# Kernel tuning notes

Measured on AMD Instinct MI355X. Metric: run time of the kernel, lower is better.

Reference implementation:

```python
import jax, jax.numpy as jnp
import numpy as np

B, D_IN, D_HID, D_OUT, N_EXP, K = 32768, 256, 512, 256, 16, 2


def setup_inputs() -> dict:
    key = jax.random.key(0)
    ks = jax.random.split(key, 5)
    s_in = 1.0 / np.sqrt(D_IN)
    s_hid = 1.0 / np.sqrt(D_HID)
    return {
        "x": jax.random.normal(ks[0], (B, D_IN), jnp.float32),
        "Wg": jax.random.normal(ks[1], (D_IN, N_EXP), jnp.float32) * s_in,
        "bg": jnp.zeros((N_EXP,), jnp.float32),
        "W1": jax.random.normal(ks[2], (N_EXP, D_IN, D_HID), jnp.float32) * s_in,
        "b1": jnp.zeros((N_EXP, D_HID), jnp.float32),
        "W2": jax.random.normal(ks[3], (N_EXP, D_HID, D_OUT), jnp.float32) * s_hid,
        "b2": jnp.zeros((N_EXP, D_OUT), jnp.float32),
    }


def reference(x, Wg, bg, W1, b1, W2, b2):
    # Gating: linear -> softmax -> top-k -> renormalize (inference path, no noise)
    logits = x @ Wg + bg                       # [B, E]
    probs = jax.nn.softmax(logits, axis=-1)
    top_w, top_idx = jax.lax.top_k(probs, K)   # [B, K]
    top_w = top_w / jnp.sum(top_w, axis=-1, keepdims=True)

    # Expert MLPs (evaluate all experts densely, then gather selected outputs;
    # same math as masked gather -> MLP -> weighted scatter-add)
    h = jax.nn.relu(jnp.einsum('bi,eih->beh', x, W1) + b1[None])  # [B, E, H]
    y_all = jnp.einsum('beh,eho->beo', h, W2) + b2[None]          # [B, E, O]

    y_sel = jnp.take_along_axis(y_all, top_idx[:, :, None], axis=1)  # [B, K, O]
    return jnp.sum(y_sel * top_w[:, :, None], axis=1)                # [B, O]
```

## Files before the change

### kernel.cpp

```cpp
#include <hip/hip_runtime.h>
#include <stdint.h>

#define BTOK 32768
#define DIN 256
#define DHID 512
#define DOUT 256
#define NEXP 16
#define BM 128
#define CH 32
#define NCH 16
#define SLOTS 96

typedef __attribute__((ext_vector_type(8))) short bf16x8;
typedef __attribute__((ext_vector_type(4))) float f32x4;

__device__ __forceinline__ unsigned short f2bf(float f){
  unsigned u = __builtin_bit_cast(unsigned, f);
  u = u + 0x7FFFu + ((u >> 16) & 1u);
  return (unsigned short)(u >> 16);
}
__device__ __forceinline__ float bf2f(unsigned short h){
  return __builtin_bit_cast(float, (unsigned)h << 16);
}
__device__ __forceinline__ void gload16(const void* g, void* l){
  __builtin_amdgcn_global_load_lds((const __attribute__((address_space(1))) unsigned int*)g,
                                   (__attribute__((address_space(3))) unsigned int*)l, 16, 0, 0);
}

__global__ __launch_bounds__(256) void transpose_cvt(const float* __restrict__ src,
                                                     unsigned short* __restrict__ dst,
                                                     int R, int C){
  __shared__ float t[32][33];
  int e = blockIdx.z, r0 = blockIdx.y * 32, c0 = blockIdx.x * 32;
  int lx = threadIdx.x & 31, ly = threadIdx.x >> 5;
  const float* s = src + (size_t)e * R * C;
  unsigned short* d = dst + (size_t)e * R * C;
#pragma unroll
  for (int i = 0; i < 4; i++){ int r = ly + i * 8; t[r][lx] = s[(size_t)(r0 + r) * C + c0 + lx]; }
  __syncthreads();
#pragma unroll
  for (int i = 0; i < 4; i++){ int r = ly + i * 8; d[(size_t)(c0 + r) * R + r0 + lx] = f2bf(t[lx][r]); }
}

__global__ __launch_bounds__(256) void transpose_cvt_w2(const float* __restrict__ src,
                                                        unsigned short* __restrict__ dst){
  __shared__ float t[32][33];
  int e = blockIdx.z, r0 = blockIdx.y * 32, c0 = blockIdx.x * 32;
  int lx = threadIdx.x & 31, ly = threadIdx.x >> 5;
  const float* s = src + (size_t)e * DHID * DOUT;
  unsigned short* d = dst + (size_t)e * DHID * DOUT + (r0 >> 5) * (DOUT * CH);
#pragma unroll
  for (int i = 0; i < 4; i++){ int r = ly + i * 8; t[r][lx] = s[(size_t)(r0 + r) * DOUT + c0 + lx]; }
  __syncthreads();
#pragma unroll
  for (int i = 0; i < 4; i++){ int rr = ly + i * 8; d[(size_t)(c0 + rr) * CH + lx] = f2bf(t[lx][rr]); }
}

__global__ __launch_bounds__(256) void gating_kernel(const float* __restrict__ x,
                                                     const float* __restrict__ Wg,
                                                     const float* __restrict__ bg,
                                                     unsigned short* __restrict__ x_bf,
                                                     int* __restrict__ top_idx,
                                                     float* __restrict__ top_w,
                                                     int* __restrict__ counts){
  __shared__ float WgT[16][256];
  __shared__ int hist[16];
  int tid = threadIdx.x;
#pragma unroll
  for (int j = 0; j < 4; j++){
    float4 wv = *(const float4*)(Wg + tid * 16 + j * 4);
    WgT[j * 4 + 0][tid] = wv.x; WgT[j * 4 + 1][tid] = wv.y;
    WgT[j * 4 + 2][tid] = wv.z; WgT[j * 4 + 3][tid] = wv.w;
  }
  if (tid < 16) hist[tid] = 0;
  __syncthreads();
  int wid = tid >> 6, lane = tid & 63;

  for (int t = 0; t < 16; t++){
    int tok = blockIdx.x * 64 + wid * 16 + t;
    const float4 xv = *(const float4*)(x + (size_t)tok * DIN + lane * 4);
    ushort4 xb; xb.x = f2bf(xv.x); xb.y = f2bf(xv.y); xb.z = f2bf(xv.z); xb.w = f2bf(xv.w);
    *(ushort4*)(x_bf + (size_t)tok * DIN + lane * 4) = xb;
    float logit[16];
#pragma unroll
    for (int e = 0; e < 16; e++){
      const float4 wv = *(const float4*)(&WgT[e][lane * 4]);
      float v = xv.x * wv.x + xv.y * wv.y + xv.z * wv.z + xv.w * wv.w;
#pragma unroll
      for (int off = 32; off; off >>= 1) v += __shfl_xor(v, off, 64);
      logit[e] = v + bg[e];
    }
    if (lane == 0){
      int i1 = 0; float v1 = logit[0];
#pragma unroll
      for (int e = 1; e < 16; e++) if (logit[e] > v1){ v1 = logit[e]; i1 = e; }
      int i2 = -1; float v2 = -3.4e38f;
#pragma unroll
      for (int e = 0; e < 16; e++) if (e != i1 && logit[e] > v2){ v2 = logit[e]; i2 = e; }
      float tt = expf(v2 - v1);
      float w1 = 1.0f / (1.0f + tt);
      float w2 = tt / (1.0f + tt);
      top_idx[tok * 2] = i1; top_idx[tok * 2 + 1] = i2;
      top_w[tok * 2] = w1;  top_w[tok * 2 + 1] = w2;
      atomicAdd(&hist[i1], 1); atomicAdd(&hist[i2], 1);
    }
  }
  __syncthreads();
  if (tid < 16) atomicAdd(&counts[tid], hist[tid]);
}

__global__ void prefix_kernel(const int* __restrict__ counts, int* __restrict__ offsets,
                              int* __restrict__ cursor, int* __restrict__ bm_e,
                              int* __restrict__ bm_start, int* __restrict__ bm_end){
  int lane = threadIdx.x & 63;
  int c = (lane < 16) ? counts[lane] : 0;
  int s = c;
#pragma unroll
  for (int off = 1; off < 16; off <<= 1){ int o = __shfl_up(s, off, 64); if (lane >= off) s += o; }
  int start = s - c;
  if (lane < 16){ offsets[lane] = start; cursor[lane] = start; }
  int nb = (c + BM - 1) >> 7;
  int nb_partner = __shfl(nb, lane ^ 8, 64);
  if (lane < 8){
    int filled = nb + nb_partner;
    if (filled > SLOTS) filled = SLOTS;
    for (int i = filled; i < SLOTS; i++) bm_e[lane * SLOTS + i] = -1;
  }
  if (lane < 16){
    int sbase = (lane < 8) ? 0 : nb_partner;
    int xcd = lane & 7;
    for (int b = 0; b < nb; b++){
      int idx = xcd * SLOTS + sbase + b;
      if (sbase + b < SLOTS){
        bm_e[idx] = lane; bm_start[idx] = start + b * BM; bm_end[idx] = start + c;
      }
    }
  }
}

__global__ __launch_bounds__(256) void scatter_kernel(const int* __restrict__ top_idx,
                                                      const float* __restrict__ top_w,
                                                      int* __restrict__ cursor,
                                                      int* __restrict__ pair_tok,
                                                      float* __restrict__ pair_w){
  __shared__ int hist[16], base[16], rank[16];
  int tid = threadIdx.x;
  if (tid < 16){ hist[tid] = 0; rank[tid] = 0; }
  __syncthreads();
  int t = blockIdx.x * 256 + tid;
  int e0 = top_idx[t * 2], e1 = top_idx[t * 2 + 1];
  float w0 = top_w[t * 2], w1 = top_w[t * 2 + 1];
  atomicAdd(&hist[e0], 1); atomicAdd(&hist[e1], 1);
  __syncthreads();
  if (tid < 16) base[tid] = atomicAdd(&cursor[tid], hist[tid]);
  __syncthreads();
  int r0 = atomicAdd(&rank[e0], 1);
  int p0 = base[e0] + r0;
  pair_tok[p0] = t; pair_w[p0] = w0;
  int r1 = atomicAdd(&rank[e1], 1);
  int p1 = base[e1] + r1;
  pair_tok[p1] = t | (1 << 16); pair_w[p1] = w1;
}

__global__ __launch_bounds__(512, 1) void moe_gemm_kernel(
    const unsigned short* __restrict__ x_bf,
    const unsigned short* __restrict__ W1t,
    const unsigned short* __restrict__ W2c,
    const float* __restrict__ b1,
    const float* __restrict__ b2,
    const int* __restrict__ pair_tok, const float* __restrict__ pair_w,
    const int* __restrict__ bm_e, const int* __restrict__ bm_start,
    const int* __restrict__ bm_end,
    unsigned short* __restrict__ ypair){
  int xcd = blockIdx.x & 7, slot = blockIdx.x >> 3;
  int bmi = xcd * SLOTS + slot;
  int e = bm_e[bmi];
  if (e < 0) return;
  int rs = bm_start[bmi], re = bm_end[bmi];

  __shared__ unsigned short w1s[3][CH * 256];
  __shared__ unsigned short w2s[3][256 * CH];
  __shared__ unsigned short hs[BM * CH];
  __shared__ float b1s[DHID];

  int tid = threadIdx.x, wid = tid >> 6, lane = tid & 63, lr = lane & 15, lh = lane >> 4;
  int mg = wid >> 1, ng = wid & 1;
  char* hsb = (char*)hs;
  const char* gW1 = (const char*)(W1t + (size_t)e * DHID * DIN);
  const char* gW2 = (const char*)(W2c + (size_t)e * DOUT * DHID);

  b1s[tid] = b1[e * DHID + tid];

  int o1 = ((tid >> 5) * 512) + (((tid & 31) ^ ((tid >> 5) & 7)) * 16);
  int o2;
  { int p = tid >> 3, q = (tid & 7) ^ (p & 7);
    o2 = (p * 2 + (q >> 2)) * 64 + (q & 3) * 16; }

#define STAGE(c, sl) {                                                    \
    const char* s1 = gW1 + (size_t)(c) * 16384;                           \
    const char* s2 = gW2 + (size_t)(c) * 16384;                           \
    char* d1 = (char*)w1s[sl]; char* d2 = (char*)w2s[sl];                 \
    gload16(s1 + o1,        d1 + tid * 16);                               \
    gload16(s1 + o1 + 8192, d1 + tid * 16 + 8192);                        \
    gload16(s2 + o2,        d2 + tid * 16);                               \
    gload16(s2 + o2 + 8192, d2 + tid * 16 + 8192);                        \
  }

  bf16x8 xr[2][8];
#pragma unroll
  for (int m = 0; m < 2; m++){
    int g0 = rs + 32 * mg + m * 16 + lr;
    int gc = g0 < re ? g0 : (re - 1);
    int tok = pair_tok[gc] & 0xFFFF;
    const unsigned short* xrow = x_bf + (size_t)tok * DIN + lh * 8;
#pragma unroll
    for (int ks = 0; ks < 8; ks++) xr[m][ks] = *(const bf16x8*)(xrow + ks * 32);
  }

  f32x4 acc[2][8];
#pragma unroll
  for (int m = 0; m < 2; m++)
#pragma unroll
    for (int i = 0; i < 8; i++) acc[m][i] = (f32x4){0.f, 0.f, 0.f, 0.f};

  STAGE(0, 0); STAGE(1, 1);
  __syncthreads();

#pragma unroll 1
  for (int c = 0; c < NCH; c++){
    int b0 = c % 3;
    if (c + 2 < NCH) STAGE(c + 2, (c + 2) % 3);

    {
      const char* w1b = (const char*)w1s[b0];
      f32x4 hacc[2];
      hacc[0] = (f32x4){0.f, 0.f, 0.f, 0.f};
      hacc[1] = (f32x4){0.f, 0.f, 0.f, 0.f};
      int hrow = 16 * ng + lr;
#pragma unroll
      for (int ks = 0; ks < 8; ks++){
        bf16x8 b = *(const bf16x8*)(w1b + ((hrow * 512 + ks * 64 + lh * 16) ^ ((hrow & 7) << 4)));
        hacc[0] = __builtin_amdgcn_mfma_f32_16x16x32_bf16(xr[0][ks], b, hacc[0], 0, 0, 0);
        hacc[1] = __builtin_amdgcn_mfma_f32_16x16x32_bf16(xr[1][ks], b, hacc[1], 0, 0, 0);
      }
      float b1v = b1s[c * CH + 16 * ng + lr];
      int col2 = (16 * ng + lr) * 2;
#pragma unroll
      for (int m = 0; m < 2; m++)
#pragma unroll
        for (int r = 0; r < 4; r++){
          int mm = 32 * mg + m * 16 + lh * 4 + r;
          float v = fmaxf(hacc[m][r] + b1v, 0.f);
          int adr = (mm >> 1) * 128 + ((((mm & 1) << 6) + col2) ^ (((mm >> 1) & 7) << 4));
          *(unsigned short*)(hsb + adr) = f2bf(v);
        }
    }
    asm volatile("s_waitcnt lgkmcnt(0)" ::: "memory");
    __builtin_amdgcn_sched_barrier(0);
    __builtin_amdgcn_s_barrier();
    __builtin_amdgcn_sched_barrier(0);

    {
      const char* w2b = (const char*)w2s[b0];
      bf16x8 ha[2];
#pragma unroll
      for (int m = 0; m < 2; m++){
        int mm = 32 * mg + m * 16 + lr;
        int hadr = (mm >> 1) * 128 + ((((mm & 1) << 6) + (lh << 4)) ^ (((mm >> 1) & 7) << 4));
        ha[m] = *(const bf16x8*)(hsb + hadr);
      }
#pragma unroll
      for (int nt = 0; nt < 8; nt++){
        int n = 128 * ng + nt * 16 + lr;
        int adr = (n >> 1) * 128 + ((((n & 1) << 6) + (lh << 4)) ^ (((n >> 1) & 7) << 4));
        bf16x8 b = *(const bf16x8*)(w2b + adr);
        acc[0][nt] = __builtin_amdgcn_mfma_f32_16x16x32_bf16(ha[0], b, acc[0][nt], 0, 0, 0);
        acc[1][nt] = __builtin_amdgcn_mfma_f32_16x16x32_bf16(ha[1], b, acc[1][nt], 0, 0, 0);
      }
    }
    if (c + 1 < NCH){
      if (c + 2 < NCH){
        asm volatile("s_waitcnt vmcnt(4) lgkmcnt(0)" ::: "memory");
      } else {
        asm volatile("s_waitcnt vmcnt(0) lgkmcnt(0)" ::: "memory");
      }
      __builtin_amdgcn_sched_barrier(0);
      __builtin_amdgcn_s_barrier();
      __builtin_amdgcn_sched_barrier(0);
    }
  }

#pragma unroll
  for (int m = 0; m < 2; m++){
    float wrow[4]; int yrow[4]; int valid[4];
#pragma unroll
    for (int r = 0; r < 4; r++){
      int gg = rs + 32 * mg + m * 16 + lh * 4 + r;
      valid[r] = gg < re;
      int gc = valid[r] ? gg : (re - 1);
      int pt = pair_tok[gc];
      yrow[r] = (pt & 0xFFFF) * 2 + (pt >> 16);
      wrow[r] = valid[r] ? pair_w[gc] : 0.f;
    }
#pragma unroll
    for (int nt = 0; nt < 8; nt++){
      int col = 128 * ng + nt * 16 + lr;
      float b2v = b2[e * DOUT + col];
#pragma unroll
      for (int r = 0; r < 4; r++){
        if (valid[r])
          ypair[(size_t)yrow[r] * DOUT + col] = f2bf(wrow[r] * (acc[m][nt][r] + b2v));
      }
    }
  }
#undef STAGE
}

__global__ __launch_bounds__(256) void combine_kernel(const unsigned short* __restrict__ yp,
                                                      float* __restrict__ out){
  int idx = blockIdx.x * 256 + threadIdx.x;
  int t = idx >> 6;
  int c4 = (idx & 63) << 2;
  ushort4 a = *(const ushort4*)(yp + (size_t)(t * 2) * DOUT + c4);
  ushort4 b = *(const ushort4*)(yp + (size_t)(t * 2 + 1) * DOUT + c4);
  float4 o;
  o.x = bf2f(a.x) + bf2f(b.x);
  o.y = bf2f(a.y) + bf2f(b.y);
  o.z = bf2f(a.z) + bf2f(b.z);
  o.w = bf2f(a.w) + bf2f(b.w);
  *(float4*)(out + (size_t)t * DOUT + c4) = o;
}

extern "C" void kernel_launch(void* const* d_in, const int* in_sizes, int n_in,
                              void* d_out, int out_size, void* d_ws, size_t ws_size,
                              hipStream_t stream){
  (void)in_sizes; (void)n_in; (void)out_size; (void)ws_size;
  const float* x  = (const float*)d_in[0];
  const float* Wg = (const float*)d_in[1];
  const float* bg = (const float*)d_in[2];
  const float* W1 = (const float*)d_in[3];
  const float* b1 = (const float*)d_in[4];
  const float* W2 = (const float*)d_in[5];
  const float* b2 = (const float*)d_in[6];
  float* out = (float*)d_out;
  char* ws = (char*)d_ws;

  unsigned short* x_bf  = (unsigned short*)(ws);
  unsigned short* W1t   = (unsigned short*)(ws + 16777216);
  unsigned short* W2ck  = (unsigned short*)(ws + 20971520);
  unsigned short* ypair = (unsigned short*)(ws + 25165824);
  int*   top_idx  = (int*)  (ws + 58720256);
  float* top_w    = (float*)(ws + 58982400);
  int*   pair_tok = (int*)  (ws + 59244544);
  float* pair_w   = (float*)(ws + 59506688);
  int*   counts   = (int*)  (ws + 60030976);
  int*   offsets  = (int*)  (ws + 60031040);
  int*   cursor   = (int*)  (ws + 60031104);
  int*   bm_e     = (int*)  (ws + 60031232);
  int*   bm_start = (int*)  (ws + 60036608);
  int*   bm_end   = (int*)  (ws + 60041984);

  hipMemsetAsync(counts, 0, 64, stream);
  transpose_cvt<<<dim3(16, 8, 16), 256, 0, stream>>>(W1, W1t, 256, 512);
  transpose_cvt_w2<<<dim3(8, 16, 16), 256, 0, stream>>>(W2, W2ck);
  gating_kernel<<<512, 256, 0, stream>>>(x, Wg, bg, x_bf, top_idx, top_w, counts);
  prefix_kernel<<<1, 64, 0, stream>>>(counts, offsets, cursor, bm_e, bm_start, bm_end);
  scatter_kernel<<<128, 256, 0, stream>>>(top_idx, top_w, cursor, pair_tok, pair_w);
  moe_gemm_kernel<<<8 * SLOTS, 512, 0, stream>>>(x_bf, W1t, W2ck, b1, b2, pair_tok, pair_w,
                                                 bm_e, bm_start, bm_end, ypair);
  combine_kernel<<<8192, 256, 0, stream>>>(ypair, out);
}
```

Before: 174.2 us.

## Halve MoE GEMM row tile, double-buffer weights, and raise occupancy

Shrinks the per-block token tile from 128 to 64 rows and raises the slot count, so roughly twice as many blocks are launched. Launch bounds now allow 4 blocks per CU. Weight staging drops from triple to double buffering, and the b1 shared-memory copy is replaced with direct global reads, which cuts LDS and register use. The goal is more resident waves to hide latency, at the cost of each block reloading the full expert weights for half as many tokens, which doubles weight traffic through the cache. The hand-tuned waitcnt and barrier sequence is replaced by plain __syncthreads.

```diff
diff --git a/kernel.cpp b/kernel.cpp
--- a/kernel.cpp
+++ b/kernel.cpp
@@ -6,10 +6,10 @@
 #define DHID 512
 #define DOUT 256
 #define NEXP 16
-#define BM 128
+#define BM 64
 #define CH 32
 #define NCH 16
-#define SLOTS 96
+#define SLOTS 168
 
 typedef __attribute__((ext_vector_type(8))) short bf16x8;
 typedef __attribute__((ext_vector_type(4))) float f32x4;
@@ -119,7 +119,7 @@
   for (int off = 1; off < 16; off <<= 1){ int o = __shfl_up(s, off, 64); if (lane >= off) s += o; }
   int start = s - c;
   if (lane < 16){ offsets[lane] = start; cursor[lane] = start; }
-  int nb = (c + BM - 1) >> 7;
+  int nb = (c + BM - 1) >> 6;
   int nb_partner = __shfl(nb, lane ^ 8, 64);
   if (lane < 8){
     int filled = nb + nb_partner;
@@ -162,7 +162,7 @@
   pair_tok[p1] = t | (1 << 16); pair_w[p1] = w1;
 }
 
-__global__ __launch_bounds__(512, 1) void moe_gemm_kernel(
+__global__ __launch_bounds__(512, 4) void moe_gemm_kernel(
     const unsigned short* __restrict__ x_bf,
     const unsigned short* __restrict__ W1t,
     const unsigned short* __restrict__ W2c,
@@ -178,18 +178,15 @@
   if (e < 0) return;
   int rs = bm_start[bmi], re = bm_end[bmi];
 
-  __shared__ unsigned short w1s[3][CH * 256];
-  __shared__ unsigned short w2s[3][256 * CH];
+  __shared__ unsigned short w1s[2][CH * 256];
+  __shared__ unsigned short w2s[2][256 * CH];
   __shared__ unsigned short hs[BM * CH];
-  __shared__ float b1s[DHID];
 
   int tid = threadIdx.x, wid = tid >> 6, lane = tid & 63, lr = lane & 15, lh = lane >> 4;
   int mg = wid >> 1, ng = wid & 1;
   char* hsb = (char*)hs;
   const char* gW1 = (const char*)(W1t + (size_t)e * DHID * DIN);
   const char* gW2 = (const char*)(W2c + (size_t)e * DOUT * DHID);
-
-  b1s[tid] = b1[e * DHID + tid];
 
   int o1 = ((tid >> 5) * 512) + (((tid & 31) ^ ((tid >> 5) & 7)) * 16);
   int o2;
@@ -206,96 +203,69 @@
     gload16(s2 + o2 + 8192, d2 + tid * 16 + 8192);                        \
   }
 
-  bf16x8 xr[2][8];
-#pragma unroll
-  for (int m = 0; m < 2; m++){
-    int g0 = rs + 32 * mg + m * 16 + lr;
+  bf16x8 xr[8];
+  {
+    int g0 = rs + 16 * mg + lr;
     int gc = g0 < re ? g0 : (re - 1);
     int tok = pair_tok[gc] & 0xFFFF;
     const unsigned short* xrow = x_bf + (size_t)tok * DIN + lh * 8;
 #pragma unroll
-    for (int ks = 0; ks < 8; ks++) xr[m][ks] = *(const bf16x8*)(xrow + ks * 32);
-  }
-
-  f32x4 acc[2][8];
-#pragma unroll
-  for (int m = 0; m < 2; m++)
-#pragma unroll
-    for (int i = 0; i < 8; i++) acc[m][i] = (f32x4){0.f, 0.f, 0.f, 0.f};
-
-  STAGE(0, 0); STAGE(1, 1);
-  __syncthreads();
-
-#pragma unroll 1
+    for (int ks = 0; ks < 8; ks++) xr[ks] = *(const bf16x8*)(xrow + ks * 32);
+  }
+
+  f32x4 acc[8];
+#pragma unroll
+  for (int i = 0; i < 8; i++) acc[i] = (f32x4){0.f, 0.f, 0.f, 0.f};
+
+  STAGE(0, 0);
+  __syncthreads();
+
   for (int c = 0; c < NCH; c++){
-    int b0 = c % 3;
-    if (c + 2 < NCH) STAGE(c + 2, (c + 2) % 3);
+    int sl = c & 1;
+    if (c + 1 < NCH) STAGE(c + 1, sl ^ 1);
 
     {
-      const char* w1b = (const char*)w1s[b0];
-      f32x4 hacc[2];
-      hacc[0] = (f32x4){0.f, 0.f, 0.f, 0.f};
-      hacc[1] = (f32x4){0.f, 0.f, 0.f, 0.f};
+      const char* w1b = (const char*)w1s[sl];
+      f32x4 hacc = (f32x4){0.f, 0.f, 0.f, 0.f};
       int hrow = 16 * ng + lr;
 #pragma unroll
       for (int ks = 0; ks < 8; ks++){
         bf16x8 b = *(const bf16x8*)(w1b + ((hrow * 512 + ks * 64 + lh * 16) ^ ((hrow & 7) << 4)));
-        hacc[0] = __builtin_amdgcn_mfma_f32_16x16x32_bf16(xr[0][ks], b, hacc[0], 0, 0, 0);
-        hacc[1] = __builtin_amdgcn_mfma_f32_16x16x32_bf16(xr[1][ks], b, hacc[1], 0, 0, 0);
-      }
-      float b1v = b1s[c * CH + 16 * ng + lr];
+        hacc = __builtin_amdgcn_mfma_f32_16x16x32_bf16(xr[ks], b, hacc, 0, 0, 0);
+      }
+      float b1v = b1[e * DHID + c * CH + 16 * ng + lr];
       int col2 = (16 * ng + lr) * 2;
 #pragma unroll
-      for (int m = 0; m < 2; m++)
-#pragma unroll
-        for (int r = 0; r < 4; r++){
-          int mm = 32 * mg + m * 16 + lh * 4 + r;
-          float v = fmaxf(hacc[m][r] + b1v, 0.f);
-          int adr = (mm >> 1) * 128 + ((((mm & 1) << 6) + col2) ^ (((mm >> 1) & 7) << 4));
-          *(unsigned short*)(hsb + adr) = f2bf(v);
-        }
-    }
-    asm volatile("s_waitcnt lgkmcnt(0)" ::: "memory");
-    __builtin_amdgcn_sched_barrier(0);
-    __builtin_amdgcn_s_barrier();
-    __builtin_amdgcn_sched_barrier(0);
+      for (int r = 0; r < 4; r++){
+        int mm = 16 * mg + lh * 4 + r;
+        float v = fmaxf(hacc[r] + b1v, 0.f);
+        int adr = (mm >> 1) * 128 + ((((mm & 1) << 6) + col2) ^ (((mm >> 1) & 7) << 4));
+        *(unsigned short*)(hsb + adr) = f2bf(v);
+      }
+    }
+    __syncthreads();
 
     {
-      const char* w2b = (const char*)w2s[b0];
-      bf16x8 ha[2];
-#pragma unroll
-      for (int m = 0; m < 2; m++){
-        int mm = 32 * mg + m * 16 + lr;
-        int hadr = (mm >> 1) * 128 + ((((mm & 1) << 6) + (lh << 4)) ^ (((mm >> 1) & 7) << 4));
-        ha[m] = *(const bf16x8*)(hsb + hadr);
-      }
+      int mm = 16 * mg + lr;
+      int hadr = (mm >> 1) * 128 + ((((mm & 1) << 6) + (lh << 4)) ^ (((mm >> 1) & 7) << 4));
+      bf16x8 ha = *(const bf16x8*)(hsb + hadr);
+      const char* w2b = (const char*)w2s[sl];
 #pragma unroll
       for (int nt = 0; nt < 8; nt++){
         int n = 128 * ng + nt * 16 + lr;
         int adr = (n >> 1) * 128 + ((((n & 1) << 6) + (lh << 4)) ^ (((n >> 1) & 7) << 4));
         bf16x8 b = *(const bf16x8*)(w2b + adr);
-        acc[0][nt] = __builtin_amdgcn_mfma_f32_16x16x32_bf16(ha[0], b, acc[0][nt], 0, 0, 0);
-        acc[1][nt] = __builtin_amdgcn_mfma_f32_16x16x32_bf16(ha[1], b, acc[1][nt], 0, 0, 0);
-      }
-    }
-    if (c + 1 < NCH){
-      if (c + 2 < NCH){
-        asm volatile("s_waitcnt vmcnt(4) lgkmcnt(0)" ::: "memory");
-      } else {
-        asm volatile("s_waitcnt vmcnt(0) lgkmcnt(0)" ::: "memory");
-      }
-      __builtin_amdgcn_sched_barrier(0);
-      __builtin_amdgcn_s_barrier();
-      __builtin_amdgcn_sched_barrier(0);
-    }
-  }
-
-#pragma unroll
-  for (int m = 0; m < 2; m++){
+        acc[nt] = __builtin_amdgcn_mfma_f32_16x16x32_bf16(ha, b, acc[nt], 0, 0, 0);
+      }
+    }
+    __syncthreads();
+  }
+
+  {
     float wrow[4]; int yrow[4]; int valid[4];
 #pragma unroll
     for (int r = 0; r < 4; r++){
-      int gg = rs + 32 * mg + m * 16 + lh * 4 + r;
+      int gg = rs + 16 * mg + lh * 4 + r;
       valid[r] = gg < re;
       int gc = valid[r] ? gg : (re - 1);
       int pt = pair_tok[gc];
@@ -309,7 +279,7 @@
 #pragma unroll
       for (int r = 0; r < 4; r++){
         if (valid[r])
-          ypair[(size_t)yrow[r] * DOUT + col] = f2bf(wrow[r] * (acc[m][nt][r] + b2v));
+          ypair[(size_t)yrow[r] * DOUT + col] = f2bf(wrow[r] * (acc[nt][r] + b2v));
       }
     }
   }
```

New measurement: 166.9 us. 1.04x faster.
